# Performance work log

Measured on AMD Instinct MI355X. Metric: run time of the kernel, lower is better.

## Reference

```python
import jax, jax.numpy as jnp
import numpy as np

D_MODEL = 1024
NUM_HEADS = 16
HEAD_DIM = D_MODEL // NUM_HEADS
BATCH, SEQ = 2, 2048


def setup_inputs() -> dict:
    key = jax.random.key(0)
    ks = jax.random.split(key, 5)
    scale = 1.0 / np.sqrt(D_MODEL)  # ~xavier magnitude
    x = jax.random.normal(ks[0], (BATCH, SEQ, D_MODEL), dtype=jnp.float32)
    Wq = jax.random.normal(ks[1], (D_MODEL, D_MODEL), dtype=jnp.float32) * scale
    Wk = jax.random.normal(ks[2], (D_MODEL, D_MODEL), dtype=jnp.float32) * scale
    Wv = jax.random.normal(ks[3], (D_MODEL, D_MODEL), dtype=jnp.float32) * scale
    Wo = jax.random.normal(ks[4], (D_MODEL, D_MODEL), dtype=jnp.float32) * scale
    z = jnp.zeros((D_MODEL,), dtype=jnp.float32)
    return {"x": x, "Wq": Wq, "bq": z, "Wk": Wk, "bk": z, "Wv": Wv, "bv": z, "Wo": Wo, "bo": z}


def reference(x, Wq, bq, Wk, bk, Wv, bv, Wo, bo):
    B, S, _ = x.shape
    H, Dh = NUM_HEADS, HEAD_DIM
    # torch Linear convention: y = x @ W^T + b
    q = (x @ Wq.T + bq).reshape(B, S, H, Dh)
    k = (x @ Wk.T + bk).reshape(B, S, H, Dh)
    v = (x @ Wv.T + bv).reshape(B, S, H, Dh)
    # scores: [B, H, S, S]
    scores = jnp.einsum('bqhd,bkhd->bhqk', q, k) / np.sqrt(Dh).astype(np.float32)
    attn = jax.nn.softmax(scores, axis=-1)
    out = jnp.einsum('bhqk,bkhd->bqhd', attn, v).reshape(B, S, H * Dh)
    return out @ Wo.T + bo
```

## Files before the change

kernel.cpp:

```cpp
#include <hip/hip_runtime.h>
#include <hip/hip_bf16.h>

typedef __bf16 bf16;
typedef __bf16 bf16x8 __attribute__((ext_vector_type(8)));
typedef __bf16 bf16x4 __attribute__((ext_vector_type(4)));
typedef float f32x4 __attribute__((ext_vector_type(4)));

constexpr int DM = 1024, NH = 16, DH = 64, NB = 2, SQ = 2048;
constexpr int MTOT = NB * SQ;
constexpr float QSCALE = 0.125f * 1.44269504088896f;

__device__ __forceinline__ void gld_lds16(const bf16* g, bf16* l) {
  __builtin_amdgcn_global_load_lds(
      (const __attribute__((address_space(1))) void*)g,
      (__attribute__((address_space(3))) void*)l, 16, 0, 0);
}

__global__ __launch_bounds__(256) void cvt5(
    const float* __restrict__ s0, const float* __restrict__ s1,
    const float* __restrict__ s2, const float* __restrict__ s3,
    const float* __restrict__ s4,
    bf16* __restrict__ d0, bf16* __restrict__ d1, bf16* __restrict__ d2,
    bf16* __restrict__ d3, bf16* __restrict__ d4) {
  const int idx = (blockIdx.x * 256 + threadIdx.x) * 4;
  const float* src; bf16* dst; int off;
  if (idx < 4 * DM * DM) {
    off = idx & (DM * DM - 1);
    switch (idx >> 20) {
      case 0: src = s0; dst = d0; break;
      case 1: src = s1; dst = d1; break;
      case 2: src = s2; dst = d2; break;
      default: src = s3; dst = d3; break;
    }
  } else {
    src = s4; dst = d4; off = idx - 4 * DM * DM;
  }
  const float4 v = *(const float4*)(src + off);
  *(bf16x4*)(dst + off) = (bf16x4){(bf16)v.x, (bf16)v.y, (bf16)v.z, (bf16)v.w};
}

template <int BM, typename OutT>
__device__ __forceinline__ void gemm_tile(
    const bf16* __restrict__ A, const bf16* __restrict__ Bm,
    const float* __restrict__ bias, OutT* __restrict__ C,
    int rowA0, int rowB0, int N, int K, bool bias_row, float cscale,
    bf16* sA, bf16* sB) {
  constexpr int NT = (BM == 128) ? 4 : 2;
  const int tid = threadIdx.x;
  const int wave = tid >> 6, lane = tid & 63;
  const int quad = lane >> 4, l16 = lane & 15;
  const int row0w = (BM == 128) ? (wave >> 1) * 64 : 0;
  const int col0w = (BM == 128) ? (wave & 1) * 64 : wave * 32;

  f32x4 acc[4][NT];
#pragma unroll
  for (int i = 0; i < 4; i++)
#pragma unroll
    for (int j = 0; j < NT; j++) acc[i][j] = (f32x4){0.f, 0.f, 0.f, 0.f};

  const int srow = lane >> 3;
  const int scol = ((lane & 7) ^ srow) * 8;

  for (int kt = 0; kt < K; kt += 64) {
#pragma unroll
    for (int i = 0; i < BM / 32; i++) {
      const int r = i * 32 + wave * 8;
      gld_lds16(A + (size_t)(rowA0 + r + srow) * K + kt + scol, &sA[r * 64]);
    }
#pragma unroll
    for (int i = 0; i < 4; i++) {
      const int r = i * 32 + wave * 8;
      gld_lds16(Bm + (size_t)(rowB0 + r + srow) * K + kt + scol, &sB[r * 64]);
    }
    __syncthreads();
#pragma unroll
    for (int kk = 0; kk < 64; kk += 32) {
      bf16x8 aF[4], bF[NT];
      const int slot = (((kk >> 3) + quad) ^ (l16 & 7)) << 3;
#pragma unroll
      for (int mt = 0; mt < 4; mt++)
        aF[mt] = *(const bf16x8*)&sA[(row0w + mt * 16 + l16) * 64 + slot];
#pragma unroll
      for (int nt = 0; nt < NT; nt++)
        bF[nt] = *(const bf16x8*)&sB[(col0w + nt * 16 + l16) * 64 + slot];
#pragma unroll
      for (int mt = 0; mt < 4; mt++)
#pragma unroll
        for (int nt = 0; nt < NT; nt++)
          acc[mt][nt] = __builtin_amdgcn_mfma_f32_16x16x32_bf16(aF[mt], bF[nt], acc[mt][nt], 0, 0, 0);
    }
    __syncthreads();
  }

#pragma unroll
  for (int mt = 0; mt < 4; mt++) {
#pragma unroll
    for (int nt = 0; nt < NT; nt++) {
#pragma unroll
      for (int r = 0; r < 4; r++) {
        const int row = rowA0 + row0w + mt * 16 + quad * 4 + r;
        const int col = rowB0 + col0w + nt * 16 + l16;
        const float bb = bias_row ? bias[row] : bias[col];
        C[(size_t)row * N + col] = (OutT)((acc[mt][nt][r] + bb) * cscale);
      }
    }
  }
}

__global__ __launch_bounds__(256, 4) void qkv_gemm(
    const bf16* __restrict__ xb, const bf16* __restrict__ Wqb,
    const bf16* __restrict__ Wkb, const bf16* __restrict__ Wvb,
    const float* __restrict__ bq, const float* __restrict__ bk,
    const float* __restrict__ bv,
    bf16* __restrict__ Qw, bf16* __restrict__ Kw, bf16* __restrict__ VTw) {
  __shared__ alignas(16) bf16 sA[128 * 64];
  __shared__ alignas(16) bf16 sB[128 * 64];
  if (blockIdx.z == 0) {
    gemm_tile<128, bf16>(xb, Wqb, bq, Qw, blockIdx.x * 128, blockIdx.y * 128, DM, DM, false, QSCALE, sA, sB);
  } else if (blockIdx.z == 1) {
    gemm_tile<128, bf16>(xb, Wkb, bk, Kw, blockIdx.x * 128, blockIdx.y * 128, DM, DM, false, 1.0f, sA, sB);
  } else {
    const int id = blockIdx.y * 32 + blockIdx.x;
    gemm_tile<128, bf16>(Wvb, xb, bv, VTw, (id >> 5) * 128, (id & 31) * 128, MTOT, DM, true, 1.0f, sA, sB);
  }
}

__global__ __launch_bounds__(256, 4) void out_gemm(
    const bf16* __restrict__ A, const bf16* __restrict__ Bm,
    const float* __restrict__ bias, float* __restrict__ C) {
  __shared__ alignas(16) bf16 sA[64 * 64];
  __shared__ alignas(16) bf16 sB[128 * 64];
  gemm_tile<64, float>(A, Bm, bias, C, blockIdx.x * 64, blockIdx.y * 128, DM, DM, false, 1.0f, sA, sB);
}

__global__ __launch_bounds__(256, 2) void attn(
    const bf16* __restrict__ Q, const bf16* __restrict__ Kq,
    const bf16* __restrict__ VT, bf16* __restrict__ O) {
  __shared__ alignas(16) bf16 sK[2][128 * 64];
  __shared__ alignas(16) bf16 sV[2][64 * 128];
  __shared__ alignas(16) bf16 sP[4][32 * 64];
  const int tid = threadIdx.x, wave = tid >> 6, lane = tid & 63;
  const int quad = lane >> 4, l16 = lane & 15;
  const int hb = blockIdx.x, qt = blockIdx.y;
  const int h = hb & 15, b = hb >> 4;

  const bf16* Qg = Q + (size_t)(b * SQ + qt * 128) * DM + h * DH;
  const bf16* Kg = Kq + (size_t)(b * SQ) * DM + h * DH;
  const bf16* Vg = VT + (size_t)(h * DH) * MTOT + b * SQ;

  const int srow = lane >> 3, scol = ((lane & 7) ^ srow) * 8;
  const int vrow = lane >> 4;

  auto stageKV = [&](int t, int buf) {
#pragma unroll
    for (int i = 0; i < 4; i++) {
      const int r = (wave * 4 + i) * 8;
      gld_lds16(Kg + (size_t)(t * 128 + r + srow) * DM + scol, &sK[buf][r * 64]);
    }
#pragma unroll
    for (int i = 0; i < 4; i++) {
      const int r = (wave * 4 + i) * 4;
      const int vchunk = (lane & 15) ^ ((r + vrow) & 7);
      gld_lds16(Vg + (size_t)(r + vrow) * MTOT + t * 128 + vchunk * 8, &sV[buf][r * 128]);
    }
  };

  bf16x8 qF[2][2];
#pragma unroll
  for (int mt = 0; mt < 2; mt++)
#pragma unroll
    for (int kkh = 0; kkh < 2; kkh++)
      qF[mt][kkh] = *(const bf16x8*)(Qg + (size_t)(wave * 32 + mt * 16 + l16) * DM +
                                     kkh * 32 + quad * 8);

  bf16x8 onesF;
#pragma unroll
  for (int i = 0; i < 8; i++) onesF[i] = (bf16)1.0f;

  f32x4 l_acc[2];
  f32x4 o_acc[2][4];
#pragma unroll
  for (int mt = 0; mt < 2; mt++) {
    l_acc[mt] = (f32x4){0.f, 0.f, 0.f, 0.f};
#pragma unroll
    for (int n2 = 0; n2 < 4; n2++) o_acc[mt][n2] = (f32x4){0.f, 0.f, 0.f, 0.f};
  }

  stageKV(0, 0);
  for (int t = 0; t < 16; ++t) {
    __syncthreads();
    if (t + 1 < 16) stageKV(t + 1, (t + 1) & 1);
    const bf16* cK = sK[t & 1];
    const bf16* cV = sV[t & 1];

    f32x4 sacc[2][8];
#pragma unroll
    for (int mt = 0; mt < 2; mt++)
#pragma unroll
      for (int nt = 0; nt < 8; nt++) sacc[mt][nt] = (f32x4){0.f, 0.f, 0.f, 0.f};
#pragma unroll
    for (int kk = 0; kk < 64; kk += 32) {
      bf16x8 kF[8];
      const int slot = (((kk >> 3) + quad) ^ (l16 & 7)) << 3;
#pragma unroll
      for (int nt = 0; nt < 8; nt++)
        kF[nt] = *(const bf16x8*)&cK[(nt * 16 + l16) * 64 + slot];
      __builtin_amdgcn_s_setprio(1);
#pragma unroll
      for (int mt = 0; mt < 2; mt++)
#pragma unroll
        for (int nt = 0; nt < 8; nt++)
          sacc[mt][nt] = __builtin_amdgcn_mfma_f32_16x16x32_bf16(kF[nt], qF[mt][kk >> 5],
                                                                 sacc[mt][nt], 0, 0, 0);
      __builtin_amdgcn_s_setprio(0);
    }

#pragma unroll
    for (int half = 0; half < 2; half++) {
#pragma unroll
      for (int mt = 0; mt < 2; mt++) {
        const int row = mt * 16 + l16;
#pragma unroll
        for (int nt4 = 0; nt4 < 4; nt4++) {
          const f32x4 s = sacc[mt][half * 4 + nt4];
          bf16x4 pk;
#pragma unroll
          for (int r = 0; r < 4; r++) pk[r] = (bf16)__builtin_amdgcn_exp2f(s[r]);
          const int c = 2 * nt4 + (quad >> 1);
          *(bf16x4*)&sP[wave][row * 64 + ((c ^ (row & 7)) << 3) + (quad & 1) * 4] = pk;
        }
      }
#pragma unroll
      for (int kk = 0; kk < 64; kk += 32) {
        bf16x8 pF[2], vF[4];
#pragma unroll
        for (int mt = 0; mt < 2; mt++) {
          const int row = mt * 16 + l16;
          const int c = (kk >> 3) + quad;
          pF[mt] = *(const bf16x8*)&sP[wave][row * 64 + ((c ^ (row & 7)) << 3)];
        }
#pragma unroll
        for (int n2 = 0; n2 < 4; n2++) {
          const int ch = ((half * 64 + kk) >> 3) + quad;
          vF[n2] = *(const bf16x8*)&cV[(n2 * 16 + l16) * 128 + ((ch ^ (l16 & 7)) << 3)];
        }
        __builtin_amdgcn_s_setprio(1);
#pragma unroll
        for (int mt = 0; mt < 2; mt++) {
#pragma unroll
          for (int n2 = 0; n2 < 4; n2++)
            o_acc[mt][n2] = __builtin_amdgcn_mfma_f32_16x16x32_bf16(pF[mt], vF[n2],
                                                                    o_acc[mt][n2], 0, 0, 0);
          l_acc[mt] = __builtin_amdgcn_mfma_f32_16x16x32_bf16(pF[mt], onesF, l_acc[mt], 0, 0, 0);
        }
        __builtin_amdgcn_s_setprio(0);
      }
    }
  }

#pragma unroll
  for (int mt = 0; mt < 2; mt++) {
#pragma unroll
    for (int r = 0; r < 4; r++) {
      const float inv = 1.0f / l_acc[mt][r];
      const int row = qt * 128 + wave * 32 + mt * 16 + quad * 4 + r;
#pragma unroll
      for (int n2 = 0; n2 < 4; n2++) {
        const int col = n2 * 16 + l16;
        O[(size_t)(b * SQ + row) * DM + h * DH + col] = (bf16)(o_acc[mt][n2][r] * inv);
      }
    }
  }
}

extern "C" void kernel_launch(void* const* d_in, const int* in_sizes, int n_in,
                              void* d_out, int out_size, void* d_ws, size_t ws_size,
                              hipStream_t stream) {
  const float* x  = (const float*)d_in[0];
  const float* Wq = (const float*)d_in[1];
  const float* bq = (const float*)d_in[2];
  const float* Wk = (const float*)d_in[3];
  const float* bk = (const float*)d_in[4];
  const float* Wv = (const float*)d_in[5];
  const float* bv = (const float*)d_in[6];
  const float* Wo = (const float*)d_in[7];
  const float* bo = (const float*)d_in[8];
  float* out = (float*)d_out;

  bf16* ws   = (bf16*)d_ws;
  bf16* xb   = ws;
  bf16* Wqb  = ws + (size_t)MTOT * DM;
  bf16* Wkb  = Wqb + (size_t)DM * DM;
  bf16* Wvb  = Wkb + (size_t)DM * DM;
  bf16* Wob  = Wvb + (size_t)DM * DM;
  bf16* Qw   = Wob + (size_t)DM * DM;
  bf16* Kw   = Qw + (size_t)MTOT * DM;
  bf16* VTw  = Kw + (size_t)MTOT * DM;
  bf16* Cw   = VTw + (size_t)MTOT * DM;

  const dim3 blk(256);
  cvt5<<<dim3((4 * DM * DM + MTOT * DM) / 1024, 1), blk, 0, stream>>>(
      Wq, Wk, Wv, Wo, x, Wqb, Wkb, Wvb, Wob, xb);
  qkv_gemm<<<dim3(32, 8, 3), blk, 0, stream>>>(xb, Wqb, Wkb, Wvb, bq, bk, bv, Qw, Kw, VTw);
  attn<<<dim3(NH * NB, SQ / 128), blk, 0, stream>>>(Qw, Kw, VTw, Cw);
  out_gemm<<<dim3(MTOT / 64, DM / 128), blk, 0, stream>>>(Cw, Wob, bo, out);
}
```

Before: 185.6 us.

## Shrink attention tiles to 64 query rows and 64-key blocks

The attention kernel now processes 64 query rows per block (16 per wave) and 64-key K/V tiles instead of 128, doubling the grid and halving LDS and register use per block. Occupancy is raised to 4 blocks per SM via launch bounds. This is meant to improve latency hiding and fill more CUs on the machine. The cost is that each K/V tile is reused by fewer queries, so global/L2 K/V traffic doubles, and there are twice as many barrier iterations.

```diff
diff --git a/kernel.cpp b/kernel.cpp
--- a/kernel.cpp
+++ b/kernel.cpp
@@ -133,142 +133,112 @@
   gemm_tile<64, float>(A, Bm, bias, C, blockIdx.x * 64, blockIdx.y * 128, DM, DM, false, 1.0f, sA, sB);
 }
 
-__global__ __launch_bounds__(256, 2) void attn(
+__global__ __launch_bounds__(256, 4) void attn(
     const bf16* __restrict__ Q, const bf16* __restrict__ Kq,
     const bf16* __restrict__ VT, bf16* __restrict__ O) {
-  __shared__ alignas(16) bf16 sK[2][128 * 64];
-  __shared__ alignas(16) bf16 sV[2][64 * 128];
-  __shared__ alignas(16) bf16 sP[4][32 * 64];
+  __shared__ alignas(16) bf16 sK[2][64 * 64];
+  __shared__ alignas(16) bf16 sV[2][64 * 64];
+  __shared__ alignas(16) bf16 sP[4][16 * 64];
   const int tid = threadIdx.x, wave = tid >> 6, lane = tid & 63;
   const int quad = lane >> 4, l16 = lane & 15;
   const int hb = blockIdx.x, qt = blockIdx.y;
   const int h = hb & 15, b = hb >> 4;
 
-  const bf16* Qg = Q + (size_t)(b * SQ + qt * 128) * DM + h * DH;
+  const bf16* Qg = Q + (size_t)(b * SQ + qt * 64) * DM + h * DH;
   const bf16* Kg = Kq + (size_t)(b * SQ) * DM + h * DH;
   const bf16* Vg = VT + (size_t)(h * DH) * MTOT + b * SQ;
 
   const int srow = lane >> 3, scol = ((lane & 7) ^ srow) * 8;
-  const int vrow = lane >> 4;
 
   auto stageKV = [&](int t, int buf) {
 #pragma unroll
-    for (int i = 0; i < 4; i++) {
-      const int r = (wave * 4 + i) * 8;
-      gld_lds16(Kg + (size_t)(t * 128 + r + srow) * DM + scol, &sK[buf][r * 64]);
-    }
-#pragma unroll
-    for (int i = 0; i < 4; i++) {
-      const int r = (wave * 4 + i) * 4;
-      const int vchunk = (lane & 15) ^ ((r + vrow) & 7);
-      gld_lds16(Vg + (size_t)(r + vrow) * MTOT + t * 128 + vchunk * 8, &sV[buf][r * 128]);
+    for (int i = 0; i < 2; i++) {
+      const int r = (wave * 2 + i) * 8;
+      gld_lds16(Kg + (size_t)(t * 64 + r + srow) * DM + scol, &sK[buf][r * 64]);
+    }
+#pragma unroll
+    for (int i = 0; i < 2; i++) {
+      const int r = (wave * 2 + i) * 8;
+      gld_lds16(Vg + (size_t)(r + srow) * MTOT + t * 64 + scol, &sV[buf][r * 64]);
     }
   };
 
-  bf16x8 qF[2][2];
-#pragma unroll
-  for (int mt = 0; mt < 2; mt++)
-#pragma unroll
-    for (int kkh = 0; kkh < 2; kkh++)
-      qF[mt][kkh] = *(const bf16x8*)(Qg + (size_t)(wave * 32 + mt * 16 + l16) * DM +
-                                     kkh * 32 + quad * 8);
+  bf16x8 qF[2];
+#pragma unroll
+  for (int kkh = 0; kkh < 2; kkh++)
+    qF[kkh] = *(const bf16x8*)(Qg + (size_t)(wave * 16 + l16) * DM + kkh * 32 + quad * 8);
 
   bf16x8 onesF;
 #pragma unroll
   for (int i = 0; i < 8; i++) onesF[i] = (bf16)1.0f;
 
-  f32x4 l_acc[2];
-  f32x4 o_acc[2][4];
-#pragma unroll
-  for (int mt = 0; mt < 2; mt++) {
-    l_acc[mt] = (f32x4){0.f, 0.f, 0.f, 0.f};
-#pragma unroll
-    for (int n2 = 0; n2 < 4; n2++) o_acc[mt][n2] = (f32x4){0.f, 0.f, 0.f, 0.f};
-  }
+  f32x4 l_acc = (f32x4){0.f, 0.f, 0.f, 0.f};
+  f32x4 o_acc[4];
+#pragma unroll
+  for (int n2 = 0; n2 < 4; n2++) o_acc[n2] = (f32x4){0.f, 0.f, 0.f, 0.f};
 
   stageKV(0, 0);
-  for (int t = 0; t < 16; ++t) {
+  for (int t = 0; t < 32; ++t) {
     __syncthreads();
-    if (t + 1 < 16) stageKV(t + 1, (t + 1) & 1);
+    if (t + 1 < 32) stageKV(t + 1, (t + 1) & 1);
     const bf16* cK = sK[t & 1];
     const bf16* cV = sV[t & 1];
 
-    f32x4 sacc[2][8];
-#pragma unroll
-    for (int mt = 0; mt < 2; mt++)
-#pragma unroll
-      for (int nt = 0; nt < 8; nt++) sacc[mt][nt] = (f32x4){0.f, 0.f, 0.f, 0.f};
+    f32x4 sacc[4];
+#pragma unroll
+    for (int nt = 0; nt < 4; nt++) sacc[nt] = (f32x4){0.f, 0.f, 0.f, 0.f};
 #pragma unroll
     for (int kk = 0; kk < 64; kk += 32) {
-      bf16x8 kF[8];
+      bf16x8 kF[4];
       const int slot = (((kk >> 3) + quad) ^ (l16 & 7)) << 3;
 #pragma unroll
-      for (int nt = 0; nt < 8; nt++)
+      for (int nt = 0; nt < 4; nt++)
         kF[nt] = *(const bf16x8*)&cK[(nt * 16 + l16) * 64 + slot];
       __builtin_amdgcn_s_setprio(1);
 #pragma unroll
-      for (int mt = 0; mt < 2; mt++)
-#pragma unroll
-        for (int nt = 0; nt < 8; nt++)
-          sacc[mt][nt] = __builtin_amdgcn_mfma_f32_16x16x32_bf16(kF[nt], qF[mt][kk >> 5],
-                                                                 sacc[mt][nt], 0, 0, 0);
+      for (int nt = 0; nt < 4; nt++)
+        sacc[nt] = __builtin_amdgcn_mfma_f32_16x16x32_bf16(kF[nt], qF[kk >> 5],
+                                                           sacc[nt], 0, 0, 0);
       __builtin_amdgcn_s_setprio(0);
     }
 
-#pragma unroll
-    for (int half = 0; half < 2; half++) {
-#pragma unroll
-      for (int mt = 0; mt < 2; mt++) {
-        const int row = mt * 16 + l16;
-#pragma unroll
-        for (int nt4 = 0; nt4 < 4; nt4++) {
-          const f32x4 s = sacc[mt][half * 4 + nt4];
-          bf16x4 pk;
-#pragma unroll
-          for (int r = 0; r < 4; r++) pk[r] = (bf16)__builtin_amdgcn_exp2f(s[r]);
-          const int c = 2 * nt4 + (quad >> 1);
-          *(bf16x4*)&sP[wave][row * 64 + ((c ^ (row & 7)) << 3) + (quad & 1) * 4] = pk;
-        }
-      }
-#pragma unroll
-      for (int kk = 0; kk < 64; kk += 32) {
-        bf16x8 pF[2], vF[4];
-#pragma unroll
-        for (int mt = 0; mt < 2; mt++) {
-          const int row = mt * 16 + l16;
-          const int c = (kk >> 3) + quad;
-          pF[mt] = *(const bf16x8*)&sP[wave][row * 64 + ((c ^ (row & 7)) << 3)];
-        }
-#pragma unroll
-        for (int n2 = 0; n2 < 4; n2++) {
-          const int ch = ((half * 64 + kk) >> 3) + quad;
-          vF[n2] = *(const bf16x8*)&cV[(n2 * 16 + l16) * 128 + ((ch ^ (l16 & 7)) << 3)];
-        }
-        __builtin_amdgcn_s_setprio(1);
-#pragma unroll
-        for (int mt = 0; mt < 2; mt++) {
-#pragma unroll
-          for (int n2 = 0; n2 < 4; n2++)
-            o_acc[mt][n2] = __builtin_amdgcn_mfma_f32_16x16x32_bf16(pF[mt], vF[n2],
-                                                                    o_acc[mt][n2], 0, 0, 0);
-          l_acc[mt] = __builtin_amdgcn_mfma_f32_16x16x32_bf16(pF[mt], onesF, l_acc[mt], 0, 0, 0);
-        }
-        __builtin_amdgcn_s_setprio(0);
-      }
-    }
-  }
-
-#pragma unroll
-  for (int mt = 0; mt < 2; mt++) {
-#pragma unroll
-    for (int r = 0; r < 4; r++) {
-      const float inv = 1.0f / l_acc[mt][r];
-      const int row = qt * 128 + wave * 32 + mt * 16 + quad * 4 + r;
-#pragma unroll
-      for (int n2 = 0; n2 < 4; n2++) {
-        const int col = n2 * 16 + l16;
-        O[(size_t)(b * SQ + row) * DM + h * DH + col] = (bf16)(o_acc[mt][n2][r] * inv);
-      }
+    const int prow = l16;
+#pragma unroll
+    for (int nt = 0; nt < 4; nt++) {
+      const f32x4 s = sacc[nt];
+      bf16x4 pk;
+#pragma unroll
+      for (int r = 0; r < 4; r++) pk[r] = (bf16)__builtin_amdgcn_exp2f(s[r]);
+      const int c = 2 * nt + (quad >> 1);
+      *(bf16x4*)&sP[wave][prow * 64 + ((c ^ (prow & 7)) << 3) + (quad & 1) * 4] = pk;
+    }
+
+#pragma unroll
+    for (int kk = 0; kk < 64; kk += 32) {
+      bf16x8 pF, vF[4];
+      const int c = (kk >> 3) + quad;
+      pF = *(const bf16x8*)&sP[wave][prow * 64 + ((c ^ (prow & 7)) << 3)];
+      const int slot = (((kk >> 3) + quad) ^ (l16 & 7)) << 3;
+#pragma unroll
+      for (int n2 = 0; n2 < 4; n2++)
+        vF[n2] = *(const bf16x8*)&cV[(n2 * 16 + l16) * 64 + slot];
+      __builtin_amdgcn_s_setprio(1);
+#pragma unroll
+      for (int n2 = 0; n2 < 4; n2++)
+        o_acc[n2] = __builtin_amdgcn_mfma_f32_16x16x32_bf16(pF, vF[n2], o_acc[n2], 0, 0, 0);
+      l_acc = __builtin_amdgcn_mfma_f32_16x16x32_bf16(pF, onesF, l_acc, 0, 0, 0);
+      __builtin_amdgcn_s_setprio(0);
+    }
+  }
+
+#pragma unroll
+  for (int r = 0; r < 4; r++) {
+    const float inv = 1.0f / l_acc[r];
+    const int row = qt * 64 + wave * 16 + quad * 4 + r;
+#pragma unroll
+    for (int n2 = 0; n2 < 4; n2++) {
+      const int col = n2 * 16 + l16;
+      O[(size_t)(b * SQ + row) * DM + h * DH + col] = (bf16)(o_acc[n2][r] * inv);
     }
   }
 }
@@ -302,6 +272,6 @@
   cvt5<<<dim3((4 * DM * DM + MTOT * DM) / 1024, 1), blk, 0, stream>>>(
       Wq, Wk, Wv, Wo, x, Wqb, Wkb, Wvb, Wob, xb);
   qkv_gemm<<<dim3(32, 8, 3), blk, 0, stream>>>(xb, Wqb, Wkb, Wvb, bq, bk, bv, Qw, Kw, VTw);
-  attn<<<dim3(NH * NB, SQ / 128), blk, 0, stream>>>(Qw, Kw, VTw, Cw);
+  attn<<<dim3(NH * NB, SQ / 64), blk, 0, stream>>>(Qw, Kw, VTw, Cw);
   out_gemm<<<dim3(MTOT / 64, DM / 128), blk, 0, stream>>>(Cw, Wob, bo, out);
 }
```

After: 188.1 us. No clear change (+1.3%).
